# Kernel tuning notes

Hardware: AMD Instinct MI355X
Metric: run time of the kernel (lower is better)

The kernel has to match this reference:

```python
import jax, jax.numpy as jnp
import numpy as np


def setup_inputs() -> dict:
    key = jax.random.key(0)
    k1, k2 = jax.random.split(key)
    inputs = jax.random.normal(k1, (64, 16, 64, 512), dtype=jnp.float32)
    cluster_centers = jax.random.normal(k2, (64, 512), dtype=jnp.float32) * 0.05
    return {"inputs": inputs, "cluster_centers": cluster_centers}


def reference(inputs, cluster_centers):
    # inputs: (B, H, W, C); cluster_centers: (K, C)
    B, H, W, C = inputs.shape
    K = cluster_centers.shape[0]
    x = inputs.reshape(B, H * W, C)                      # (B, N, C)
    # soft assignments: softmax over K of x @ centers^T
    logits = jnp.einsum('bnc,kc->bnk', x, cluster_centers)
    a = jax.nn.softmax(logits, axis=-1)                  # (B, N, K)
    # VLAD rewritten to avoid (B,N,K,C) residual tensor:
    # sum_n a[b,n,k] * (x[b,n,:] - c[k,:])
    #   = (a^T @ x)[b,k,:] - (sum_n a[b,n,k]) * c[k,:]
    agg = jnp.einsum('bnk,bnc->bkc', a, x)               # (B, K, C)
    a_sum = jnp.sum(a, axis=1)                           # (B, K)
    vlad = agg - a_sum[:, :, None] * cluster_centers[None, :, :]
    vlad = vlad.reshape(B, K * C)
    # tf.nn.l2_normalize: x / sqrt(max(sum(x^2), eps)), eps=1e-12
    norm = jnp.sqrt(jnp.maximum(jnp.sum(vlad * vlad, axis=-1, keepdims=True), 1e-12))
    return vlad / norm
```

## Files before the change

kernel.cpp:

```cpp
#include <hip/hip_runtime.h>
#include <stdint.h>

#define NB 64
#define NN 1024
#define CDIM 512
#define KK 64

typedef __attribute__((ext_vector_type(4))) float f32x4;
typedef __attribute__((ext_vector_type(8))) short short8;

__device__ __forceinline__ unsigned short f2bf(float f) {
  unsigned int u = __float_as_uint(f);
  return (unsigned short)((u + 0x7fffu + ((u >> 16) & 1u)) >> 16);
}
__device__ __forceinline__ float bf2f(unsigned short h) {
  return __uint_as_float(((unsigned int)h) << 16);
}

__device__ __forceinline__ void lgkm_barrier() {
  asm volatile("s_waitcnt lgkmcnt(0)" ::: "memory");
  __builtin_amdgcn_sched_barrier(0);
  __builtin_amdgcn_s_barrier();
}

__global__ __launch_bounds__(256) void k0_cvt(const float* __restrict__ cc,
                                              unsigned short* __restrict__ ccb) {
  int i = blockIdx.x * 256 + threadIdx.x;
  ccb[i] = f2bf(cc[i]);
}

__global__ __launch_bounds__(256, 1) void k1_assign(const float* __restrict__ x,
    const unsigned short* __restrict__ ccb, unsigned int* __restrict__ a_t32,
    unsigned int* __restrict__ xT32) {
  const int b = blockIdx.y;
  const int tid = threadIdx.x;
  const int w = tid >> 6;
  const int l = tid & 63;
  const int lr = l & 15;
  const int lg = l >> 4;
  const int n0 = ((blockIdx.x << 2) + w) << 6;
  const int codd = l & 1;

  __shared__ unsigned int xsw_all[4][32 * 33];
  __shared__ unsigned int asw_all[4][64 * 33];
  unsigned int* xsw = xsw_all[w];
  unsigned int* asw = asw_all[w];

  const float* xr = x + ((size_t)b * NN + n0 + lr) * CDIM + (lg << 3);
  const unsigned short* cb = ccb + lr * CDIM + (lg << 3);

  f32x4 acc[4][4];
  #pragma unroll
  for (int i = 0; i < 4; ++i)
    #pragma unroll
    for (int j = 0; j < 4; ++j) acc[i][j] = (f32x4){0.f, 0.f, 0.f, 0.f};

  #pragma unroll 2
  for (int step = 0; step < 16; ++step) {
    const int cs = step << 5;
    short8 af[4];
    #pragma unroll
    for (int tn = 0; tn < 4; ++tn) {
      f32x4 xa = *(const f32x4*)(xr + (size_t)(tn << 4) * CDIM + cs);
      f32x4 xb = *(const f32x4*)(xr + (size_t)(tn << 4) * CDIM + cs + 4);
      short8 t;
      t[0] = (short)f2bf(xa[0]); t[1] = (short)f2bf(xa[1]);
      t[2] = (short)f2bf(xa[2]); t[3] = (short)f2bf(xa[3]);
      t[4] = (short)f2bf(xb[0]); t[5] = (short)f2bf(xb[1]);
      t[6] = (short)f2bf(xb[2]); t[7] = (short)f2bf(xb[3]);
      af[tn] = t;
    }
    short8 bq0 = *(const short8*)(cb + cs);
    short8 bq1 = *(const short8*)(cb + 16 * CDIM + cs);
    short8 bq2 = *(const short8*)(cb + 32 * CDIM + cs);
    short8 bq3 = *(const short8*)(cb + 48 * CDIM + cs);
    #pragma unroll
    for (int tn = 0; tn < 4; ++tn) {
      acc[tn][0] = __builtin_amdgcn_mfma_f32_16x16x32_bf16(af[tn], bq0, acc[tn][0], 0, 0, 0);
      acc[tn][1] = __builtin_amdgcn_mfma_f32_16x16x32_bf16(af[tn], bq1, acc[tn][1], 0, 0, 0);
      acc[tn][2] = __builtin_amdgcn_mfma_f32_16x16x32_bf16(af[tn], bq2, acc[tn][2], 0, 0, 0);
      acc[tn][3] = __builtin_amdgcn_mfma_f32_16x16x32_bf16(af[tn], bq3, acc[tn][3], 0, 0, 0);
    }
    #pragma unroll
    for (int tn = 0; tn < 4; ++tn) {
      #pragma unroll
      for (int q = 0; q < 4; ++q) {
        unsigned int own = ((const unsigned int*)&af[tn])[q];
        unsigned int oth = (unsigned int)__shfl_xor((int)own, 1);
        unsigned int v = codd ? ((oth >> 16) | (own & 0xffff0000u))
                              : ((own & 0xffffu) | (oth << 16));
        xsw[((lg << 3) + (q << 1) + codd) * 33 + (tn << 3) + (lr >> 1)] = v;
      }
    }
    #pragma unroll
    for (int i = 0; i < 16; ++i) {
      const int row = (i << 1) + (l >> 5);
      xT32[(((size_t)((b << 9) + cs + row)) << 9) + (n0 >> 1) + (l & 31)] =
          xsw[row * 33 + (l & 31)];
    }
  }

  #pragma unroll
  for (int tn = 0; tn < 4; ++tn) {
    #pragma unroll
    for (int j = 0; j < 4; ++j) {
      float m = fmaxf(fmaxf(acc[tn][0][j], acc[tn][1][j]),
                      fmaxf(acc[tn][2][j], acc[tn][3][j]));
      m = fmaxf(m, __shfl_xor(m, 1));
      m = fmaxf(m, __shfl_xor(m, 2));
      m = fmaxf(m, __shfl_xor(m, 4));
      m = fmaxf(m, __shfl_xor(m, 8));
      float e0 = __expf(acc[tn][0][j] - m);
      float e1 = __expf(acc[tn][1][j] - m);
      float e2 = __expf(acc[tn][2][j] - m);
      float e3 = __expf(acc[tn][3][j] - m);
      float s = e0 + e1 + e2 + e3;
      s += __shfl_xor(s, 1); s += __shfl_xor(s, 2);
      s += __shfl_xor(s, 4); s += __shfl_xor(s, 8);
      float inv = 1.0f / s;
      acc[tn][0][j] = e0 * inv;
      acc[tn][1][j] = e1 * inv;
      acc[tn][2][j] = e2 * inv;
      acc[tn][3][j] = e3 * inv;
    }
  }
  #pragma unroll
  for (int tn = 0; tn < 4; ++tn)
    #pragma unroll
    for (int tk = 0; tk < 4; ++tk)
      #pragma unroll
      for (int jp = 0; jp < 2; ++jp) {
        unsigned int v = (unsigned int)f2bf(acc[tn][tk][2 * jp]) |
                         ((unsigned int)f2bf(acc[tn][tk][2 * jp + 1]) << 16);
        asw[((tk << 4) + lr) * 33 + (tn << 3) + (lg << 1) + jp] = v;
      }
  #pragma unroll
  for (int i = 0; i < 32; ++i) {
    const int k = (i << 1) + (l >> 5);
    a_t32[(((size_t)((b << 6) + k)) << 9) + (n0 >> 1) + (l & 31)] =
        asw[k * 33 + (l & 31)];
  }
}

#define XRS 38
__global__ __launch_bounds__(256) void k2_agg(
    const unsigned short* __restrict__ a_t, const unsigned int* __restrict__ xT32,
    const float* __restrict__ cc, float* __restrict__ out,
    float* __restrict__ sumsq) {
  const int b = blockIdx.y;
  const int c0 = blockIdx.x << 6;
  const int tid = threadIdx.x;
  const int w = tid >> 6;
  const int l = tid & 63;
  const int lr = l & 15;
  const int lg = l >> 4;

  __shared__ unsigned int xs[2][64 * XRS];
  __shared__ float red[4];

  f32x4 acc[4];
  #pragma unroll
  for (int i = 0; i < 4; ++i) acc[i] = (f32x4){0.f, 0.f, 0.f, 0.f};
  float ssum = 0.f;

  const unsigned short* ap =
      a_t + (((size_t)((b << 6) + (w << 4) + lr)) << 10) + (lg << 3);
  const unsigned int* xg =
      xT32 + (((size_t)((b << 9) + c0 + (tid >> 5))) << 9) + (tid & 31);

  #pragma unroll
  for (int p = 0; p < 8; ++p) {
    const int f = (p << 8) + tid;
    xs[0][(f >> 5) * XRS + (f & 31)] = xg[(((size_t)p) << 12)];
  }
  short8 a_cur0 = *(const short8*)(ap);
  short8 a_cur1 = *(const short8*)(ap + 32);
  lgkm_barrier();

  for (int it = 0; it < 16; ++it) {
    const int cur = it & 1;
    unsigned int xr[8];
    short8 a_nxt0, a_nxt1;
    if (it < 15) {
      const int nu = (it + 1) << 5;
      #pragma unroll
      for (int p = 0; p < 8; ++p) xr[p] = xg[(((size_t)p) << 12) + nu];
      a_nxt0 = *(const short8*)(ap + ((it + 1) << 6));
      a_nxt1 = *(const short8*)(ap + ((it + 1) << 6) + 32);
    }
    #pragma unroll
    for (int i = 0; i < 8; ++i)
      ssum += bf2f((unsigned short)a_cur0[i]) + bf2f((unsigned short)a_cur1[i]);
    #pragma unroll
    for (int ns = 0; ns < 64; ns += 32) {
      const short8 af = ns == 0 ? a_cur0 : a_cur1;
      #pragma unroll
      for (int ct = 0; ct < 4; ++ct) {
        const int row = (ct << 4) + lr;
        const unsigned long long* bp = (const unsigned long long*)
            &xs[cur][row * XRS + (ns >> 1) + (lg << 2)];
        union { unsigned long long q[2]; short8 s; } u;
        u.q[0] = bp[0];
        u.q[1] = bp[1];
        acc[ct] = __builtin_amdgcn_mfma_f32_16x16x32_bf16(af, u.s, acc[ct], 0, 0, 0);
      }
    }
    if (it < 15) {
      #pragma unroll
      for (int p = 0; p < 8; ++p) {
        const int f = (p << 8) + tid;
        xs[cur ^ 1][(f >> 5) * XRS + (f & 31)] = xr[p];
      }
      a_cur0 = a_nxt0;
      a_cur1 = a_nxt1;
    }
    lgkm_barrier();
  }

  ssum += __shfl_xor(ssum, 16);
  ssum += __shfl_xor(ssum, 32);

  float lsum = 0.f;
  #pragma unroll
  for (int j = 0; j < 4; ++j) {
    const float asum_e = __shfl(ssum, (lg << 2) + j);
    #pragma unroll
    for (int ct = 0; ct < 4; ++ct) {
      int k = (w << 4) + (lg << 2) + j;
      int c = c0 + (ct << 4) + lr;
      float v = acc[ct][j] - asum_e * cc[k * CDIM + c];
      out[((size_t)b << 15) + (k << 9) + c] = v;
      lsum += v * v;
    }
  }
  lsum += __shfl_xor(lsum, 1);  lsum += __shfl_xor(lsum, 2);
  lsum += __shfl_xor(lsum, 4);  lsum += __shfl_xor(lsum, 8);
  lsum += __shfl_xor(lsum, 16); lsum += __shfl_xor(lsum, 32);
  if (l == 0) red[w] = lsum;
  __syncthreads();
  if (tid == 0) atomicAdd(&sumsq[b], red[0] + red[1] + red[2] + red[3]);
}

__global__ __launch_bounds__(256) void k3_norm(float* __restrict__ out,
                                               const float* __restrict__ sumsq) {
  int idx = blockIdx.x * 256 + threadIdx.x;
  int b = idx >> 13;
  float s = sumsq[b];
  float scale = 1.0f / sqrtf(fmaxf(s, 1e-12f));
  f32x4* io = (f32x4*)out;
  f32x4 v = io[idx];
  v[0] *= scale; v[1] *= scale; v[2] *= scale; v[3] *= scale;
  io[idx] = v;
}

extern "C" void kernel_launch(void* const* d_in, const int* in_sizes, int n_in,
                              void* d_out, int out_size, void* d_ws, size_t ws_size,
                              hipStream_t stream) {
  const float* x  = (const float*)d_in[0];
  const float* cc = (const float*)d_in[1];
  float* out = (float*)d_out;
  char* ws = (char*)d_ws;
  unsigned short* a_t = (unsigned short*)ws;
  unsigned int* a_t32 = (unsigned int*)ws;
  unsigned short* ccb = (unsigned short*)(ws + (8u << 20));
  float* sumsq = (float*)(ws + (8u << 20) + (64u << 10));
  unsigned int* xT32 = (unsigned int*)(ws + (16u << 20));

  (void)hipMemsetAsync(sumsq, 0, NB * 4, stream);
  k0_cvt<<<dim3((KK * CDIM) / 256), 256, 0, stream>>>(cc, ccb);
  k1_assign<<<dim3(4, NB), 256, 0, stream>>>(x, ccb, a_t32, xT32);
  k2_agg<<<dim3(8, NB), 256, 0, stream>>>(a_t, xT32, cc, out, sumsq);
  k3_norm<<<dim3(2048), 256, 0, stream>>>(out, sumsq);
}
```

Baseline: 79.08 us.

## Halve k1 tile per wave, double grid, write transposed x directly to global

k1_assign now gives each wave 32 points instead of 64 and launches twice as many blocks (8x64), with launch bounds allowing two blocks per CU. The K-loop handles 64 channels per step, issuing all eight loads up front to add memory-level parallelism. The LDS staging buffer for the bf16 transposed x is removed, and each lane writes its packed pairs straight to global, which gives less coalesced stores. The assignment LDS tile shrinks to match, aiming for higher occupancy on the bandwidth-bound first pass.

```diff
diff --git a/kernel.cpp b/kernel.cpp
--- a/kernel.cpp
+++ b/kernel.cpp
@@ -29,7 +29,7 @@
   ccb[i] = f2bf(cc[i]);
 }
 
-__global__ __launch_bounds__(256, 1) void k1_assign(const float* __restrict__ x,
+__global__ __launch_bounds__(256, 2) void k1_assign(const float* __restrict__ x,
     const unsigned short* __restrict__ ccb, unsigned int* __restrict__ a_t32,
     unsigned int* __restrict__ xT32) {
   const int b = blockIdx.y;
@@ -38,70 +38,80 @@
   const int l = tid & 63;
   const int lr = l & 15;
   const int lg = l >> 4;
-  const int n0 = ((blockIdx.x << 2) + w) << 6;
+  const int nc = (blockIdx.x << 2) + w;
+  const int n0 = nc << 5;
   const int codd = l & 1;
 
-  __shared__ unsigned int xsw_all[4][32 * 33];
-  __shared__ unsigned int asw_all[4][64 * 33];
-  unsigned int* xsw = xsw_all[w];
+  __shared__ unsigned int asw_all[4][64 * 17];
   unsigned int* asw = asw_all[w];
 
-  const float* xr = x + ((size_t)b * NN + n0 + lr) * CDIM + (lg << 3);
+  const float* xr0 = x + ((size_t)b * NN + n0 + lr) * CDIM + (lg << 3);
+  const float* xr1 = xr0 + (size_t)16 * CDIM;
   const unsigned short* cb = ccb + lr * CDIM + (lg << 3);
-
-  f32x4 acc[4][4];
-  #pragma unroll
-  for (int i = 0; i < 4; ++i)
+  unsigned int* xTb = xT32 + (((size_t)b) << 18) + (n0 >> 1) + (lr >> 1)
+                      + (((size_t)((lg << 3) + codd)) << 9);
+
+  f32x4 acc[2][4];
+  #pragma unroll
+  for (int i = 0; i < 2; ++i)
     #pragma unroll
     for (int j = 0; j < 4; ++j) acc[i][j] = (f32x4){0.f, 0.f, 0.f, 0.f};
 
   #pragma unroll 2
-  for (int step = 0; step < 16; ++step) {
-    const int cs = step << 5;
-    short8 af[4];
-    #pragma unroll
-    for (int tn = 0; tn < 4; ++tn) {
-      f32x4 xa = *(const f32x4*)(xr + (size_t)(tn << 4) * CDIM + cs);
-      f32x4 xb = *(const f32x4*)(xr + (size_t)(tn << 4) * CDIM + cs + 4);
-      short8 t;
-      t[0] = (short)f2bf(xa[0]); t[1] = (short)f2bf(xa[1]);
-      t[2] = (short)f2bf(xa[2]); t[3] = (short)f2bf(xa[3]);
-      t[4] = (short)f2bf(xb[0]); t[5] = (short)f2bf(xb[1]);
-      t[6] = (short)f2bf(xb[2]); t[7] = (short)f2bf(xb[3]);
-      af[tn] = t;
-    }
-    short8 bq0 = *(const short8*)(cb + cs);
-    short8 bq1 = *(const short8*)(cb + 16 * CDIM + cs);
-    short8 bq2 = *(const short8*)(cb + 32 * CDIM + cs);
-    short8 bq3 = *(const short8*)(cb + 48 * CDIM + cs);
-    #pragma unroll
-    for (int tn = 0; tn < 4; ++tn) {
-      acc[tn][0] = __builtin_amdgcn_mfma_f32_16x16x32_bf16(af[tn], bq0, acc[tn][0], 0, 0, 0);
-      acc[tn][1] = __builtin_amdgcn_mfma_f32_16x16x32_bf16(af[tn], bq1, acc[tn][1], 0, 0, 0);
-      acc[tn][2] = __builtin_amdgcn_mfma_f32_16x16x32_bf16(af[tn], bq2, acc[tn][2], 0, 0, 0);
-      acc[tn][3] = __builtin_amdgcn_mfma_f32_16x16x32_bf16(af[tn], bq3, acc[tn][3], 0, 0, 0);
-    }
-    #pragma unroll
-    for (int tn = 0; tn < 4; ++tn) {
-      #pragma unroll
-      for (int q = 0; q < 4; ++q) {
-        unsigned int own = ((const unsigned int*)&af[tn])[q];
-        unsigned int oth = (unsigned int)__shfl_xor((int)own, 1);
-        unsigned int v = codd ? ((oth >> 16) | (own & 0xffff0000u))
-                              : ((own & 0xffffu) | (oth << 16));
-        xsw[((lg << 3) + (q << 1) + codd) * 33 + (tn << 3) + (lr >> 1)] = v;
-      }
-    }
-    #pragma unroll
-    for (int i = 0; i < 16; ++i) {
-      const int row = (i << 1) + (l >> 5);
-      xT32[(((size_t)((b << 9) + cs + row)) << 9) + (n0 >> 1) + (l & 31)] =
-          xsw[row * 33 + (l & 31)];
-    }
-  }
-
-  #pragma unroll
-  for (int tn = 0; tn < 4; ++tn) {
+  for (int step = 0; step < 8; ++step) {
+    const int cs = step << 6;
+    f32x4 xa00 = *(const f32x4*)(xr0 + cs);
+    f32x4 xb00 = *(const f32x4*)(xr0 + cs + 4);
+    f32x4 xa01 = *(const f32x4*)(xr0 + cs + 32);
+    f32x4 xb01 = *(const f32x4*)(xr0 + cs + 36);
+    f32x4 xa10 = *(const f32x4*)(xr1 + cs);
+    f32x4 xb10 = *(const f32x4*)(xr1 + cs + 4);
+    f32x4 xa11 = *(const f32x4*)(xr1 + cs + 32);
+    f32x4 xb11 = *(const f32x4*)(xr1 + cs + 36);
+    short8 af[2][2];
+    #pragma unroll
+    for (int tn = 0; tn < 2; ++tn) {
+      #pragma unroll
+      for (int sub = 0; sub < 2; ++sub) {
+        const f32x4 xa = tn == 0 ? (sub == 0 ? xa00 : xa01)
+                                 : (sub == 0 ? xa10 : xa11);
+        const f32x4 xb = tn == 0 ? (sub == 0 ? xb00 : xb01)
+                                 : (sub == 0 ? xb10 : xb11);
+        short8 t;
+        t[0] = (short)f2bf(xa[0]); t[1] = (short)f2bf(xa[1]);
+        t[2] = (short)f2bf(xa[2]); t[3] = (short)f2bf(xa[3]);
+        t[4] = (short)f2bf(xb[0]); t[5] = (short)f2bf(xb[1]);
+        t[6] = (short)f2bf(xb[2]); t[7] = (short)f2bf(xb[3]);
+        af[tn][sub] = t;
+      }
+    }
+    #pragma unroll
+    for (int tk = 0; tk < 4; ++tk) {
+      short8 bq0 = *(const short8*)(cb + tk * 16 * CDIM + cs);
+      short8 bq1 = *(const short8*)(cb + tk * 16 * CDIM + cs + 32);
+      acc[0][tk] = __builtin_amdgcn_mfma_f32_16x16x32_bf16(af[0][0], bq0, acc[0][tk], 0, 0, 0);
+      acc[0][tk] = __builtin_amdgcn_mfma_f32_16x16x32_bf16(af[0][1], bq1, acc[0][tk], 0, 0, 0);
+      acc[1][tk] = __builtin_amdgcn_mfma_f32_16x16x32_bf16(af[1][0], bq0, acc[1][tk], 0, 0, 0);
+      acc[1][tk] = __builtin_amdgcn_mfma_f32_16x16x32_bf16(af[1][1], bq1, acc[1][tk], 0, 0, 0);
+    }
+    #pragma unroll
+    for (int tn = 0; tn < 2; ++tn) {
+      #pragma unroll
+      for (int sub = 0; sub < 2; ++sub) {
+        #pragma unroll
+        for (int q = 0; q < 4; ++q) {
+          unsigned int own = ((const unsigned int*)&af[tn][sub])[q];
+          unsigned int oth = (unsigned int)__shfl_xor((int)own, 1);
+          unsigned int v = codd ? ((oth >> 16) | (own & 0xffff0000u))
+                                : ((own & 0xffffu) | (oth << 16));
+          xTb[(((size_t)(cs + (sub << 5) + (q << 1))) << 9) + (tn << 3)] = v;
+        }
+      }
+    }
+  }
+
+  #pragma unroll
+  for (int tn = 0; tn < 2; ++tn) {
     #pragma unroll
     for (int j = 0; j < 4; ++j) {
       float m = fmaxf(fmaxf(acc[tn][0][j], acc[tn][1][j]),
@@ -125,20 +135,20 @@
     }
   }
   #pragma unroll
-  for (int tn = 0; tn < 4; ++tn)
+  for (int tn = 0; tn < 2; ++tn)
     #pragma unroll
     for (int tk = 0; tk < 4; ++tk)
       #pragma unroll
       for (int jp = 0; jp < 2; ++jp) {
         unsigned int v = (unsigned int)f2bf(acc[tn][tk][2 * jp]) |
                          ((unsigned int)f2bf(acc[tn][tk][2 * jp + 1]) << 16);
-        asw[((tk << 4) + lr) * 33 + (tn << 3) + (lg << 1) + jp] = v;
-      }
-  #pragma unroll
-  for (int i = 0; i < 32; ++i) {
-    const int k = (i << 1) + (l >> 5);
-    a_t32[(((size_t)((b << 6) + k)) << 9) + (n0 >> 1) + (l & 31)] =
-        asw[k * 33 + (l & 31)];
+        asw[((tk << 4) + lr) * 17 + (tn << 3) + (lg << 1) + jp] = v;
+      }
+  #pragma unroll
+  for (int i = 0; i < 16; ++i) {
+    const int k = (i << 2) + (l >> 4);
+    const int np = l & 15;
+    a_t32[(((size_t)((b << 6) + k)) << 9) + (n0 >> 1) + np] = asw[k * 17 + np];
   }
 }
 
@@ -268,7 +278,7 @@
 
   (void)hipMemsetAsync(sumsq, 0, NB * 4, stream);
   k0_cvt<<<dim3((KK * CDIM) / 256), 256, 0, stream>>>(cc, ccb);
-  k1_assign<<<dim3(4, NB), 256, 0, stream>>>(x, ccb, a_t32, xT32);
+  k1_assign<<<dim3(8, NB), 256, 0, stream>>>(x, ccb, a_t32, xT32);
   k2_agg<<<dim3(8, NB), 256, 0, stream>>>(a_t, xT32, cc, out, sumsq);
   k3_norm<<<dim3(2048), 256, 0, stream>>>(out, sumsq);
 }
```

Measured after the change: 82.19 us. 1.04x slower.
